# Kernel tuning notes

Measured on AMD Instinct MI355X. Metric: run time of the kernel, lower is better.

The kernel has to match this reference:

```python
import jax, jax.numpy as jnp
import numpy as np

NW, OBS, HS, HS2, HM, CTX, ACT = 2048, 512, 512, 512, 256, 128, 18


def setup_inputs() -> dict:
    key = jax.random.key(0)
    ks = jax.random.split(key, 20)
    s = 0.02  # small init so tanh/softmax/sigmoid stay in sane range
    f32 = jnp.float32
    return {
        "obs": jax.random.normal(ks[0], (NW, 1, OBS), f32),
        "hidden_memory": jax.random.normal(ks[1], (1, NW, HM), f32),
        # fnn: Linear(obs_size, hidden_size)
        "W1": (jax.random.normal(ks[2], (HS, OBS), f32) * s),
        "b1": jnp.zeros((HS,), f32),
        # context: Linear(hidden_memory_size + 1, context_size)
        "Wc": (jax.random.normal(ks[3], (CTX, HM + 1), f32) * s),
        "bc": jnp.zeros((CTX,), f32),
        # attention: Linear(context_size, 1)
        "Wa": (jax.random.normal(ks[4], (1, CTX), f32) * s),
        "ba": jnp.zeros((1,), f32),
        # GRU(input=1, hidden=HM)
        "W_ih": (jax.random.normal(ks[5], (3 * HM, 1), f32) * s),
        "b_ih": jnp.zeros((3 * HM,), f32),
        "W_hh": (jax.random.normal(ks[6], (3 * HM, HM), f32) * s),
        "b_hh": jnp.zeros((3 * HM,), f32),
        # fnn2: Linear(hidden_size + hidden_memory_size, hidden_size_2)
        "W2": (jax.random.normal(ks[7], (HS2, HS + HM), f32) * s),
        "b2": jnp.zeros((HS2,), f32),
        # actor / critic heads
        "Wact": (jax.random.normal(ks[8], (ACT, HS2), f32) * s),
        "bact": jnp.zeros((ACT,), f32),
        "Wcrit": (jax.random.normal(ks[9], (1, HS2), f32) * s),
        "bcrit": jnp.zeros((1,), f32),
    }


def reference(obs, hidden_memory, W1, b1, Wc, bc, Wa, ba,
              W_ih, b_ih, W_hh, b_hh, W2, b2, Wact, bact, Wcrit, bcrit):
    # obs: [NW, 1, OBS], hidden_memory: [1, NW, HM]
    feat = jax.nn.relu(jnp.einsum('bto,ho->bth', obs, W1) + b1)  # [NW,1,HS]

    # context: Linear([obs_scalar, hidden_memory]) + tanh.
    # Split the (HM+1)-dim contraction: col 0 multiplies the obs scalar,
    # cols 1: contract with the broadcast hidden memory (same math as the
    # torch cat + Linear, without materializing the [NW,1,OBS,HM+1] tensor).
    h = jnp.swapaxes(hidden_memory, 0, 1)                        # [NW,1,HM]
    h_term = jnp.einsum('btm,cm->btc', h, Wc[:, 1:]) + bc        # [NW,1,CTX]
    ctx = jnp.tanh(obs[..., None] * Wc[:, 0] + h_term[:, :, None, :])  # [NW,1,OBS,CTX]

    # attention: Linear(CTX -> 1) then softmax over the obs dimension (dim=-2
    # of [...,OBS,1] == OBS after squeeze)
    alog = jnp.einsum('btoc,c->bto', ctx, Wa[0]) + ba[0]         # [NW,1,OBS]
    attn = jax.nn.softmax(alog, axis=-1)
    dset = jnp.sum(attn * obs, axis=-1, keepdims=True)           # [NW,1,1]

    # single-step GRU (torch gate ordering: r, z, n)
    x = dset[:, 0, :]                                            # [NW,1]
    hp = hidden_memory[0]                                        # [NW,HM]
    gi = x @ W_ih.T + b_ih                                       # [NW,3HM]
    gh = hp @ W_hh.T + b_hh
    ir, iz, inn = jnp.split(gi, 3, axis=-1)
    hr, hz, hn = jnp.split(gh, 3, axis=-1)
    r = jax.nn.sigmoid(ir + hr)
    z = jax.nn.sigmoid(iz + hz)
    n = jnp.tanh(inn + r * hn)
    hnew = (1.0 - z) * n + z * hp                                # [NW,HM]

    out = jnp.concatenate([feat[:, 0, :], hnew], axis=-1)        # [NW,HS+HM]
    out = jax.nn.relu(out @ W2.T + b2)                           # [NW,HS2]
    logits = out @ Wact.T + bact                                 # [NW,ACT]
    action = jax.random.categorical(jax.random.key(42), logits)  # [NW]
    log_prob = jax.nn.log_softmax(logits)[jnp.arange(logits.shape[0]), action]
    value = out @ Wcrit.T + bcrit                                # [NW,1]
    return (action, value, log_prob)
```

## Files before the change

kernel.cpp:

```cpp
#include <hip/hip_runtime.h>
#include <stdint.h>

#define NW   2048
#define OBS  512
#define HS   512
#define HS2  512
#define HM   256
#define CTX  128
#define ACT  18

#define K2LE 2.8853900817779268f

#define W1T_OFF   0
#define WCT_OFF   262144
#define W2T_OFF   294912
#define WHHQ_OFF  688128
#define FEAT_OFF  950272
#define GATES_OFF 1998848
#define HTERM_OFF 3571712
#define X_OFF     3833856

#if __has_builtin(__builtin_amdgcn_exp2f)
#define EXP2F(x) __builtin_amdgcn_exp2f(x)
#else
#define EXP2F(x) exp2f(x)
#endif
#if __has_builtin(__builtin_amdgcn_rcpf)
#define RCPF(x) __builtin_amdgcn_rcpf(x)
#else
#define RCPF(x) (1.0f/(x))
#endif

#define TFR(x0, x1, R) { x0 += x1; x1 = (x1 << R) | (x1 >> (32 - R)); x1 ^= x0; }

__device__ __forceinline__ void threefry_0_42(uint32_t x0, uint32_t x1,
                                              uint32_t& o0, uint32_t& o1) {
    const uint32_t ks0 = 0u;
    const uint32_t ks1 = 42u;
    const uint32_t ks2 = 0x1BD11BDAu ^ ks0 ^ ks1;
    x0 += ks0; x1 += ks1;
    TFR(x0, x1, 13) TFR(x0, x1, 15) TFR(x0, x1, 26) TFR(x0, x1, 6)
    x0 += ks1; x1 += ks2 + 1u;
    TFR(x0, x1, 17) TFR(x0, x1, 29) TFR(x0, x1, 16) TFR(x0, x1, 24)
    x0 += ks2; x1 += ks0 + 2u;
    TFR(x0, x1, 13) TFR(x0, x1, 15) TFR(x0, x1, 26) TFR(x0, x1, 6)
    x0 += ks0; x1 += ks1 + 3u;
    TFR(x0, x1, 17) TFR(x0, x1, 29) TFR(x0, x1, 16) TFR(x0, x1, 24)
    x0 += ks1; x1 += ks2 + 4u;
    TFR(x0, x1, 13) TFR(x0, x1, 15) TFR(x0, x1, 26) TFR(x0, x1, 6)
    x0 += ks2; x1 += ks0 + 5u;
    o0 = x0; o1 = x1;
}

__device__ __forceinline__ float gumbel_ra(int row, int a) {
    uint32_t n = (uint32_t)(row * ACT + a);
    uint32_t o0, o1;
    threefry_0_42(0u, n, o0, o1);
    uint32_t bits = o0 ^ o1;
    uint32_t fb = (bits >> 9) | 0x3F800000u;
    float f = __uint_as_float(fb) - 1.0f;
    const float tiny = 1.17549435e-38f;
    float u = (f < tiny) ? tiny : f;
    return -logf(-logf(u));
}

__device__ __forceinline__ float fast_tanh(float x) {
    float e = __expf(2.0f * x);
    return 1.0f - 2.0f / (e + 1.0f);
}
__device__ __forceinline__ float fast_sig(float x) {
    return 1.0f / (1.0f + __expf(-x));
}

__global__ __launch_bounds__(256) void transpose_weights(
    const float* __restrict__ W1, const float* __restrict__ Wc,
    const float* __restrict__ Whh, const float* __restrict__ W2,
    float* __restrict__ ws)
{
    __shared__ float t[3][32][33];
    const int tx = threadIdx.x & 31, ty = threadIdx.x >> 5;
    int b = blockIdx.x;
    if (b < 672) {
        const float* src; float* dst; int ld, off, R, it, jt;
        if (b < 256)      { src = W1;  dst = ws + W1T_OFF;  ld = 512; off = 0; it = b >> 4; jt = b & 15; R = 512; }
        else if (b < 288) { int bb = b - 256; src = Wc;  dst = ws + WCT_OFF;  ld = 257; off = 1; it = bb >> 3; jt = bb & 7;  R = 128; }
        else              { int bb = b - 288; src = W2;  dst = ws + W2T_OFF;  ld = 768; off = 0; it = bb / 24; jt = bb % 24; R = 512; }
        const int i0 = it * 32, j0 = jt * 32;
        #pragma unroll
        for (int q = 0; q < 4; ++q)
            t[0][ty + 8 * q][tx] = src[(i0 + ty + 8 * q) * ld + off + j0 + tx];
        __syncthreads();
        #pragma unroll
        for (int q = 0; q < 4; ++q)
            dst[(j0 + ty + 8 * q) * R + i0 + tx] = t[0][tx][ty + 8 * q];
    } else {
        int bb = b - 672;
        const int mt = bb >> 3, jt = bb & 7;
        const int m0 = mt * 32, j0 = jt * 32;
        #pragma unroll
        for (int g = 0; g < 3; ++g)
            #pragma unroll
            for (int q = 0; q < 4; ++q)
                t[g][ty + 8 * q][tx] = Whh[(g * HM + j0 + ty + 8 * q) * HM + m0 + tx];
        __syncthreads();
        float4* dst = (float4*)(ws + WHHQ_OFF);
        #pragma unroll
        for (int q = 0; q < 4; ++q) {
            int ml = ty + 8 * q, jl = tx;
            dst[(size_t)(m0 + ml) * HM + j0 + jl] =
                make_float4(t[0][jl][ml], t[1][jl][ml], t[2][jl][ml], 0.0f);
        }
    }
}

__global__ __launch_bounds__(256) void gemm8(
    const float* __restrict__ obs, const float* __restrict__ hmem,
    const float* __restrict__ b1,  const float* __restrict__ bc,
    const float* __restrict__ bhh, float* __restrict__ ws)
{
    __shared__ float s_act[8 * 512];
    const int tid = threadIdx.x;
    const int wv = tid >> 6, lane = tid & 63;
    const int bid = blockIdx.x;

    if (bid < 256) {
        const int m0 = bid * 8;
        for (int i = tid; i < 1024; i += 256) {
            int r = i >> 7, kq = i & 127;
            *(float4*)&s_act[r * 512 + kq * 4] =
                *(const float4*)&obs[(size_t)(m0 + r) * 512 + kq * 4];
        }
        __syncthreads();
        const float2* __restrict__ Wt = (const float2*)(ws + W1T_OFF);
        const int c2 = wv * 64 + lane;
        float2 acc[8];
        #pragma unroll
        for (int r = 0; r < 8; ++r) acc[r] = make_float2(0.f, 0.f);
        #pragma unroll 4
        for (int k = 0; k < 512; k += 4) {
            float2 w0 = Wt[(k + 0) * 256 + c2];
            float2 w1 = Wt[(k + 1) * 256 + c2];
            float2 w2 = Wt[(k + 2) * 256 + c2];
            float2 w3 = Wt[(k + 3) * 256 + c2];
            #pragma unroll
            for (int r = 0; r < 8; ++r) {
                float4 o = *(const float4*)&s_act[r * 512 + k];
                acc[r].x = fmaf(o.x, w0.x, acc[r].x); acc[r].y = fmaf(o.x, w0.y, acc[r].y);
                acc[r].x = fmaf(o.y, w1.x, acc[r].x); acc[r].y = fmaf(o.y, w1.y, acc[r].y);
                acc[r].x = fmaf(o.z, w2.x, acc[r].x); acc[r].y = fmaf(o.z, w2.y, acc[r].y);
                acc[r].x = fmaf(o.w, w3.x, acc[r].x); acc[r].y = fmaf(o.w, w3.y, acc[r].y);
            }
        }
        float2 bb = ((const float2*)b1)[c2];
        float* F = ws + FEAT_OFF;
        #pragma unroll
        for (int r = 0; r < 8; ++r) {
            float2 v;
            v.x = fmaxf(acc[r].x + bb.x, 0.f);
            v.y = fmaxf(acc[r].y + bb.y, 0.f);
            *(float2*)&F[(size_t)(m0 + r) * 512 + c2 * 2] = v;
        }
    } else if (bid < 512) {
        const int m0 = (bid - 256) * 8;
        for (int i = tid; i < 512; i += 256) {
            int r = i >> 6, kq = i & 63;
            *(float4*)&s_act[r * 256 + kq * 4] =
                *(const float4*)&hmem[(size_t)(m0 + r) * 256 + kq * 4];
        }
        __syncthreads();
        const float4* __restrict__ Q = (const float4*)(ws + WHHQ_OFF);
        const int j = wv * 64 + lane;
        float ar[8] = {0,0,0,0,0,0,0,0}, az[8] = {0,0,0,0,0,0,0,0}, an[8] = {0,0,0,0,0,0,0,0};
        #pragma unroll 4
        for (int k = 0; k < 256; k += 4) {
            float4 q0 = Q[(k + 0) * 256 + j];
            float4 q1 = Q[(k + 1) * 256 + j];
            float4 q2 = Q[(k + 2) * 256 + j];
            float4 q3 = Q[(k + 3) * 256 + j];
            #pragma unroll
            for (int r = 0; r < 8; ++r) {
                float4 h = *(const float4*)&s_act[r * 256 + k];
                ar[r] = fmaf(h.x, q0.x, ar[r]); az[r] = fmaf(h.x, q0.y, az[r]); an[r] = fmaf(h.x, q0.z, an[r]);
                ar[r] = fmaf(h.y, q1.x, ar[r]); az[r] = fmaf(h.y, q1.y, az[r]); an[r] = fmaf(h.y, q1.z, an[r]);
                ar[r] = fmaf(h.z, q2.x, ar[r]); az[r] = fmaf(h.z, q2.y, az[r]); an[r] = fmaf(h.z, q2.z, an[r]);
                ar[r] = fmaf(h.w, q3.x, ar[r]); az[r] = fmaf(h.w, q3.y, az[r]); an[r] = fmaf(h.w, q3.z, an[r]);
            }
        }
        float br = bhh[j], bz = bhh[HM + j], bn = bhh[2 * HM + j];
        float* G = ws + GATES_OFF;
        #pragma unroll
        for (int r = 0; r < 8; ++r) {
            size_t base = (size_t)(m0 + r) * 768 + j;
            G[base]       = ar[r] + br;
            G[base + 256] = az[r] + bz;
            G[base + 512] = an[r] + bn;
        }
    } else {
        const int m0 = (bid - 512) * 8;
        for (int i = tid; i < 512; i += 256) {
            int r = i >> 6, kq = i & 63;
            *(float4*)&s_act[r * 256 + kq * 4] =
                *(const float4*)&hmem[(size_t)(m0 + r) * 256 + kq * 4];
        }
        __syncthreads();
        const float2* __restrict__ Wt = (const float2*)(ws + WCT_OFF);
        const int r0 = wv * 2;
        float2 a0 = make_float2(0.f, 0.f), a1 = make_float2(0.f, 0.f);
        #pragma unroll 4
        for (int k = 0; k < 256; k += 4) {
            float2 w0 = Wt[(k + 0) * 64 + lane];
            float2 w1 = Wt[(k + 1) * 64 + lane];
            float2 w2 = Wt[(k + 2) * 64 + lane];
            float2 w3 = Wt[(k + 3) * 64 + lane];
            float4 o0 = *(const float4*)&s_act[r0 * 256 + k];
            float4 o1 = *(const float4*)&s_act[(r0 + 1) * 256 + k];
            a0.x = fmaf(o0.x, w0.x, a0.x); a0.y = fmaf(o0.x, w0.y, a0.y);
            a0.x = fmaf(o0.y, w1.x, a0.x); a0.y = fmaf(o0.y, w1.y, a0.y);
            a0.x = fmaf(o0.z, w2.x, a0.x); a0.y = fmaf(o0.z, w2.y, a0.y);
            a0.x = fmaf(o0.w, w3.x, a0.x); a0.y = fmaf(o0.w, w3.y, a0.y);
            a1.x = fmaf(o1.x, w0.x, a1.x); a1.y = fmaf(o1.x, w0.y, a1.y);
            a1.x = fmaf(o1.y, w1.x, a1.x); a1.y = fmaf(o1.y, w1.y, a1.y);
            a1.x = fmaf(o1.z, w2.x, a1.x); a1.y = fmaf(o1.z, w2.y, a1.y);
            a1.x = fmaf(o1.w, w3.x, a1.x); a1.y = fmaf(o1.w, w3.y, a1.y);
        }
        float2 bb = ((const float2*)bc)[lane];
        float* H = ws + HTERM_OFF;
        float2 v0, v1;
        v0.x = K2LE * (a0.x + bb.x); v0.y = K2LE * (a0.y + bb.y);
        v1.x = K2LE * (a1.x + bb.x); v1.y = K2LE * (a1.y + bb.y);
        *(float2*)&H[(size_t)(m0 + r0) * 128 + lane * 2]     = v0;
        *(float2*)&H[(size_t)(m0 + r0 + 1) * 128 + lane * 2] = v1;
    }
}

__global__ __launch_bounds__(512) void attn_kernel(
    const float* __restrict__ obs, const float* __restrict__ Wc,
    const float* __restrict__ Wa,  const float* __restrict__ ba,
    float* __restrict__ ws)
{
    __shared__ float s_obs[4][512];
    __shared__ float s_ht[4][128];
    __shared__ float s_alog[4][512];
    __shared__ float s_wc0[128], s_wa2[128];

    const int tid = threadIdx.x;
    const int row0 = blockIdx.x * 4;
    const float* hterm = ws + HTERM_OFF;
    float* X = ws + X_OFF;

    {
        int r = tid >> 7, kq = tid & 127;
        *(float4*)&s_obs[r][kq * 4] =
            *(const float4*)&obs[(size_t)(row0 + r) * 512 + kq * 4];
    }
    if (tid < 128) {
        int r = tid >> 5, kq = tid & 31;
        *(float4*)&s_ht[r][kq * 4] =
            *(const float4*)&hterm[(size_t)(row0 + r) * 128 + kq * 4];
    } else if (tid < 256) {
        int t = tid - 128;
        s_wc0[t] = K2LE * Wc[t * (HM + 1)];
        s_wa2[t] = 2.0f * Wa[t];
    }
    __syncthreads();

    {
        const float ba0 = ba[0];
        const int o = tid;
        float ob[4], acA[4];
        #pragma unroll
        for (int r = 0; r < 4; ++r) { ob[r] = s_obs[r][o]; acA[r] = 0.f; }
        float swa = 0.f;
        for (int c = 0; c < 128; c += 4) {
            float4 v = *(const float4*)&s_wa2[c];
            swa += v.x + v.y + v.z + v.w;
        }
        swa *= 0.5f;
        for (int c4 = 0; c4 < 32; ++c4) {
            float4 wc = *(const float4*)&s_wc0[c4 * 4];
            float4 wa = *(const float4*)&s_wa2[c4 * 4];
            #pragma unroll
            for (int r = 0; r < 4; ++r) {
                float4 ht = *(const float4*)&s_ht[r][c4 * 4];
                float t0 = fmaf(ob[r], wc.x, ht.x);
                acA[r] = fmaf(wa.x, RCPF(EXP2F(t0) + 1.f), acA[r]);
                float t1 = fmaf(ob[r], wc.y, ht.y);
                acA[r] = fmaf(wa.y, RCPF(EXP2F(t1) + 1.f), acA[r]);
                float t2 = fmaf(ob[r], wc.z, ht.z);
                acA[r] = fmaf(wa.z, RCPF(EXP2F(t2) + 1.f), acA[r]);
                float t3 = fmaf(ob[r], wc.w, ht.w);
                acA[r] = fmaf(wa.w, RCPF(EXP2F(t3) + 1.f), acA[r]);
            }
        }
        #pragma unroll
        for (int r = 0; r < 4; ++r) s_alog[r][o] = ba0 + swa - acA[r];
    }
    __syncthreads();

    {
        const int wv = tid >> 6, lane = tid & 63;
        if (wv < 4) {
            const int r = wv;
            float m = -1e30f;
            for (int o = lane; o < 512; o += 64) m = fmaxf(m, s_alog[r][o]);
            #pragma unroll
            for (int d = 32; d >= 1; d >>= 1) m = fmaxf(m, __shfl_xor(m, d));
            float se = 0.f, sw = 0.f;
            for (int o = lane; o < 512; o += 64) {
                float e = __expf(s_alog[r][o] - m);
                se += e; sw += e * s_obs[r][o];
            }
            #pragma unroll
            for (int d = 32; d >= 1; d >>= 1) { se += __shfl_xor(se, d); sw += __shfl_xor(sw, d); }
            if (lane == 0) X[row0 + r] = sw / se;
        }
    }
}

__global__ __launch_bounds__(512) void out2_heads(
    const float* __restrict__ hmem,  const float* __restrict__ W_ih,
    const float* __restrict__ b_ih,  const float* __restrict__ b2,
    const float* __restrict__ Wact,  const float* __restrict__ bact,
    const float* __restrict__ Wcrit, const float* __restrict__ bcrit,
    const float* __restrict__ ws,    float* __restrict__ out)
{
    __shared__ float s_act[8 * 768];
    __shared__ float s_P[8 * 512];
    const int tid = threadIdx.x;
    const int wv = tid >> 6, lane = tid & 63;
    const int m0 = blockIdx.x * 8;
    const float* F = ws + FEAT_OFF;
    const float* G = ws + GATES_OFF;
    const float* X = ws + X_OFF;

    for (int i = tid; i < 1024; i += 512) {
        int r = i >> 7, kq = i & 127;
        *(float4*)&s_act[r * 768 + kq * 4] =
            *(const float4*)&F[(size_t)(m0 + r) * 512 + kq * 4];
    }
    for (int i = tid; i < 2048; i += 512) {
        int r = i >> 8, j = i & 255;
        int grow = m0 + r;
        float g0 = G[(size_t)grow * 768 + j];
        float g1 = G[(size_t)grow * 768 + 256 + j];
        float g2 = G[(size_t)grow * 768 + 512 + j];
        float hp = hmem[(size_t)grow * 256 + j];
        float x  = X[grow];
        float rg = fast_sig(fmaf(x, W_ih[j], b_ih[j]) + g0);
        float zg = fast_sig(fmaf(x, W_ih[256 + j], b_ih[256 + j]) + g1);
        float ng = fast_tanh(fmaf(x, W_ih[512 + j], b_ih[512 + j]) + rg * g2);
        s_act[r * 768 + 512 + j] = (1.0f - zg) * ng + zg * hp;
    }
    __syncthreads();

    const float2* __restrict__ Wt = (const float2*)(ws + W2T_OFF);
    const int kg = wv & 1, cg = wv >> 1;
    const int c2 = cg * 64 + lane;
    const int k0 = kg * 384;
    float2 acc[8];
    #pragma unroll
    for (int r = 0; r < 8; ++r) acc[r] = make_float2(0.f, 0.f);
    #pragma unroll 4
    for (int k = k0; k < k0 + 384; k += 4) {
        float2 w0 = Wt[(k + 0) * 256 + c2];
        float2 w1 = Wt[(k + 1) * 256 + c2];
        float2 w2 = Wt[(k + 2) * 256 + c2];
        float2 w3 = Wt[(k + 3) * 256 + c2];
        #pragma unroll
        for (int r = 0; r < 8; ++r) {
            float4 o = *(const float4*)&s_act[r * 768 + k];
            acc[r].x = fmaf(o.x, w0.x, acc[r].x); acc[r].y = fmaf(o.x, w0.y, acc[r].y);
            acc[r].x = fmaf(o.y, w1.x, acc[r].x); acc[r].y = fmaf(o.y, w1.y, acc[r].y);
            acc[r].x = fmaf(o.z, w2.x, acc[r].x); acc[r].y = fmaf(o.z, w2.y, acc[r].y);
            acc[r].x = fmaf(o.w, w3.x, acc[r].x); acc[r].y = fmaf(o.w, w3.y, acc[r].y);
        }
    }
    float2* P2 = (float2*)s_P;
    if (kg == 1) {
        #pragma unroll
        for (int r = 0; r < 8; ++r) P2[r * 256 + c2] = acc[r];
    }
    __syncthreads();
    float (*s_out)[512] = (float (*)[512])s_act;
    if (kg == 0) {
        float2 bb = ((const float2*)b2)[c2];
        #pragma unroll
        for (int r = 0; r < 8; ++r) {
            float2 p = P2[r * 256 + c2];
            float2 v;
            v.x = fmaxf(acc[r].x + p.x + bb.x, 0.f);
            v.y = fmaxf(acc[r].y + p.y + bb.y, 0.f);
            *(float2*)&s_out[r][c2 * 2] = v;
        }
    }
    __syncthreads();

    {
        const int rr = wv;
        const int grow = m0 + rr;
        float4 x0 = *(const float4*)&s_out[rr][lane * 8];
        float4 x1 = *(const float4*)&s_out[rr][lane * 8 + 4];
        float la[ACT];
        #pragma unroll
        for (int a = 0; a < ACT; ++a) {
            const float4* wa4 = (const float4*)&Wact[a * HS2 + lane * 8];
            float4 w0 = wa4[0], w1 = wa4[1];
            float p = x0.x * w0.x + x0.y * w0.y + x0.z * w0.z + x0.w * w0.w
                    + x1.x * w1.x + x1.y * w1.y + x1.z * w1.z + x1.w * w1.w;
            #pragma unroll
            for (int d = 32; d >= 1; d >>= 1) p += __shfl_xor(p, d);
            la[a] = p + bact[a];
        }
        const float4* wc4 = (const float4*)&Wcrit[lane * 8];
        float4 w0 = wc4[0], w1 = wc4[1];
        float pv = x0.x * w0.x + x0.y * w0.y + x0.z * w0.z + x0.w * w0.w
                 + x1.x * w1.x + x1.y * w1.y + x1.z * w1.z + x1.w * w1.w;
        #pragma unroll
        for (int d = 32; d >= 1; d >>= 1) pv += __shfl_xor(pv, d);

        float g = (lane < ACT) ? gumbel_ra(grow, lane) : 0.0f;
        float best = -1e30f; int amax = 0;
        float mx = -1e30f;
        #pragma unroll
        for (int a = 0; a < ACT; ++a) {
            float g_ = __shfl(g, a);
            float y = la[a] + g_;
            if (y > best) { best = y; amax = a; }
            mx = fmaxf(mx, la[a]);
        }
        float se = 0.f;
        #pragma unroll
        for (int a = 0; a < ACT; ++a) se += __expf(la[a] - mx);
        float lse = mx + logf(se);
        float lp = la[amax] - lse;
        if (lane == 0) {
            out[grow]          = (float)amax;
            out[NW + grow]     = pv + bcrit[0];
            out[2 * NW + grow] = lp;
        }
    }
}

extern "C" void kernel_launch(void* const* d_in, const int* in_sizes, int n_in,
                              void* d_out, int out_size, void* d_ws, size_t ws_size,
                              hipStream_t stream) {
    const float* obs   = (const float*)d_in[0];
    const float* hmem  = (const float*)d_in[1];
    const float* W1    = (const float*)d_in[2];
    const float* b1    = (const float*)d_in[3];
    const float* Wc    = (const float*)d_in[4];
    const float* bc    = (const float*)d_in[5];
    const float* Wa    = (const float*)d_in[6];
    const float* ba    = (const float*)d_in[7];
    const float* W_ih  = (const float*)d_in[8];
    const float* b_ih  = (const float*)d_in[9];
    const float* W_hh  = (const float*)d_in[10];
    const float* b_hh  = (const float*)d_in[11];
    const float* W2    = (const float*)d_in[12];
    const float* b2    = (const float*)d_in[13];
    const float* Wact  = (const float*)d_in[14];
    const float* bact  = (const float*)d_in[15];
    const float* Wcrit = (const float*)d_in[16];
    const float* bcrit = (const float*)d_in[17];
    float* ws = (float*)d_ws;

    transpose_weights<<<736, 256, 0, stream>>>(W1, Wc, W_hh, W2, ws);
    gemm8<<<768, 256, 0, stream>>>(obs, hmem, b1, bc, b_hh, ws);
    attn_kernel<<<512, 512, 0, stream>>>(obs, Wc, Wa, ba, ws);
    out2_heads<<<256, 512, 0, stream>>>(hmem, W_ih, b_ih, b2,
                                        Wact, bact, Wcrit, bcrit, ws, (float*)d_out);
}
```

Before: 125.8 us.

## Split out2 GEMM from heads and widen grid with column and K splitting

Measured after the change: 119.2 us. -5.3%, faster.

```diff
diff --git a/kernel.cpp b/kernel.cpp
--- a/kernel.cpp
+++ b/kernel.cpp
@@ -19,6 +19,7 @@
 #define GATES_OFF 1998848
 #define HTERM_OFF 3571712
 #define X_OFF     3833856
+#define OUT2_OFF  3835904
 
 #if __has_builtin(__builtin_amdgcn_exp2f)
 #define EXP2F(x) __builtin_amdgcn_exp2f(x)
@@ -317,21 +318,20 @@
     }
 }
 
-__global__ __launch_bounds__(512) void out2_heads(
+__global__ __launch_bounds__(512) void out2_gemm(
     const float* __restrict__ hmem,  const float* __restrict__ W_ih,
     const float* __restrict__ b_ih,  const float* __restrict__ b2,
-    const float* __restrict__ Wact,  const float* __restrict__ bact,
-    const float* __restrict__ Wcrit, const float* __restrict__ bcrit,
-    const float* __restrict__ ws,    float* __restrict__ out)
+    const float* __restrict__ ws_c,  float* __restrict__ ws)
 {
     __shared__ float s_act[8 * 768];
-    __shared__ float s_P[8 * 512];
+    __shared__ float s_P[6144];
     const int tid = threadIdx.x;
     const int wv = tid >> 6, lane = tid & 63;
-    const int m0 = blockIdx.x * 8;
-    const float* F = ws + FEAT_OFF;
-    const float* G = ws + GATES_OFF;
-    const float* X = ws + X_OFF;
+    const int rowb = blockIdx.x >> 1, colb = blockIdx.x & 1;
+    const int m0 = rowb * 8;
+    const float* F = ws_c + FEAT_OFF;
+    const float* G = ws_c + GATES_OFF;
+    const float* X = ws_c + X_OFF;
 
     for (int i = tid; i < 1024; i += 512) {
         int r = i >> 7, kq = i & 127;
@@ -353,15 +353,15 @@
     }
     __syncthreads();
 
-    const float2* __restrict__ Wt = (const float2*)(ws + W2T_OFF);
-    const int kg = wv & 1, cg = wv >> 1;
-    const int c2 = cg * 64 + lane;
-    const int k0 = kg * 384;
+    const float2* __restrict__ Wt = (const float2*)(ws_c + W2T_OFF);
+    const int kg = wv & 3, cg = wv >> 2;
+    const int c2 = colb * 128 + cg * 64 + lane;
+    const int k0 = kg * 192;
     float2 acc[8];
     #pragma unroll
     for (int r = 0; r < 8; ++r) acc[r] = make_float2(0.f, 0.f);
     #pragma unroll 4
-    for (int k = k0; k < k0 + 384; k += 4) {
+    for (int k = k0; k < k0 + 192; k += 4) {
         float2 w0 = Wt[(k + 0) * 256 + c2];
         float2 w1 = Wt[(k + 1) * 256 + c2];
         float2 w2 = Wt[(k + 2) * 256 + c2];
@@ -376,68 +376,78 @@
         }
     }
     float2* P2 = (float2*)s_P;
-    if (kg == 1) {
-        #pragma unroll
-        for (int r = 0; r < 8; ++r) P2[r * 256 + c2] = acc[r];
+    const int cl = cg * 64 + lane;
+    if (kg != 0) {
+        #pragma unroll
+        for (int r = 0; r < 8; ++r) P2[((kg - 1) * 8 + r) * 128 + cl] = acc[r];
     }
     __syncthreads();
-    float (*s_out)[512] = (float (*)[512])s_act;
     if (kg == 0) {
         float2 bb = ((const float2*)b2)[c2];
+        float* O = ws + OUT2_OFF;
         #pragma unroll
         for (int r = 0; r < 8; ++r) {
-            float2 p = P2[r * 256 + c2];
+            float2 p0 = P2[(0 * 8 + r) * 128 + cl];
+            float2 p1 = P2[(1 * 8 + r) * 128 + cl];
+            float2 p2 = P2[(2 * 8 + r) * 128 + cl];
             float2 v;
-            v.x = fmaxf(acc[r].x + p.x + bb.x, 0.f);
-            v.y = fmaxf(acc[r].y + p.y + bb.y, 0.f);
-            *(float2*)&s_out[r][c2 * 2] = v;
-        }
-    }
-    __syncthreads();
-
-    {
-        const int rr = wv;
-        const int grow = m0 + rr;
-        float4 x0 = *(const float4*)&s_out[rr][lane * 8];
-        float4 x1 = *(const float4*)&s_out[rr][lane * 8 + 4];
-        float la[ACT];
-        #pragma unroll
-        for (int a = 0; a < ACT; ++a) {
-            const float4* wa4 = (const float4*)&Wact[a * HS2 + lane * 8];
-            float4 w0 = wa4[0], w1 = wa4[1];
-            float p = x0.x * w0.x + x0.y * w0.y + x0.z * w0.z + x0.w * w0.w
-                    + x1.x * w1.x + x1.y * w1.y + x1.z * w1.z + x1.w * w1.w;
-            #pragma unroll
-            for (int d = 32; d >= 1; d >>= 1) p += __shfl_xor(p, d);
-            la[a] = p + bact[a];
-        }
-        const float4* wc4 = (const float4*)&Wcrit[lane * 8];
-        float4 w0 = wc4[0], w1 = wc4[1];
-        float pv = x0.x * w0.x + x0.y * w0.y + x0.z * w0.z + x0.w * w0.w
-                 + x1.x * w1.x + x1.y * w1.y + x1.z * w1.z + x1.w * w1.w;
-        #pragma unroll
-        for (int d = 32; d >= 1; d >>= 1) pv += __shfl_xor(pv, d);
-
-        float g = (lane < ACT) ? gumbel_ra(grow, lane) : 0.0f;
-        float best = -1e30f; int amax = 0;
-        float mx = -1e30f;
-        #pragma unroll
-        for (int a = 0; a < ACT; ++a) {
-            float g_ = __shfl(g, a);
-            float y = la[a] + g_;
-            if (y > best) { best = y; amax = a; }
-            mx = fmaxf(mx, la[a]);
-        }
-        float se = 0.f;
-        #pragma unroll
-        for (int a = 0; a < ACT; ++a) se += __expf(la[a] - mx);
-        float lse = mx + logf(se);
-        float lp = la[amax] - lse;
-        if (lane == 0) {
-            out[grow]          = (float)amax;
-            out[NW + grow]     = pv + bcrit[0];
-            out[2 * NW + grow] = lp;
-        }
+            v.x = fmaxf(acc[r].x + p0.x + p1.x + p2.x + bb.x, 0.f);
+            v.y = fmaxf(acc[r].y + p0.y + p1.y + p2.y + bb.y, 0.f);
+            *(float2*)&ws[OUT2_OFF + (size_t)(m0 + r) * 512 + c2 * 2] = v;
+        }
+        (void)O;
+    }
+}
+
+__global__ __launch_bounds__(512) void heads_kernel(
+    const float* __restrict__ Wact,  const float* __restrict__ bact,
+    const float* __restrict__ Wcrit, const float* __restrict__ bcrit,
+    const float* __restrict__ ws,    float* __restrict__ out)
+{
+    const int wv = threadIdx.x >> 6, lane = threadIdx.x & 63;
+    const int grow = blockIdx.x * 8 + wv;
+    const float* o2 = ws + OUT2_OFF;
+
+    float4 x0 = *(const float4*)&o2[(size_t)grow * 512 + lane * 8];
+    float4 x1 = *(const float4*)&o2[(size_t)grow * 512 + lane * 8 + 4];
+
+    float la[ACT];
+    #pragma unroll
+    for (int a = 0; a < ACT; ++a) {
+        const float4* wa4 = (const float4*)&Wact[a * HS2 + lane * 8];
+        float4 w0 = wa4[0], w1 = wa4[1];
+        float p = x0.x * w0.x + x0.y * w0.y + x0.z * w0.z + x0.w * w0.w
+                + x1.x * w1.x + x1.y * w1.y + x1.z * w1.z + x1.w * w1.w;
+        #pragma unroll
+        for (int d = 32; d >= 1; d >>= 1) p += __shfl_xor(p, d);
+        la[a] = p + bact[a];
+    }
+    const float4* wc4 = (const float4*)&Wcrit[lane * 8];
+    float4 w0 = wc4[0], w1 = wc4[1];
+    float pv = x0.x * w0.x + x0.y * w0.y + x0.z * w0.z + x0.w * w0.w
+             + x1.x * w1.x + x1.y * w1.y + x1.z * w1.z + x1.w * w1.w;
+    #pragma unroll
+    for (int d = 32; d >= 1; d >>= 1) pv += __shfl_xor(pv, d);
+
+    float g = (lane < ACT) ? gumbel_ra(grow, lane) : 0.0f;
+    float best = -1e30f; int amax = 0;
+    float mx = -1e30f;
+    #pragma unroll
+    for (int a = 0; a < ACT; ++a) {
+        float g_ = __shfl(g, a);
+        float y = la[a] + g_;
+        if (y > best) { best = y; amax = a; }
+        mx = fmaxf(mx, la[a]);
+    }
+    float se = 0.f;
+    #pragma unroll
+    for (int a = 0; a < ACT; ++a) se += __expf(la[a] - mx);
+    float lse = mx + logf(se);
+    float lp = la[amax] - lse;
+    if (lane == 0) {
+        out[grow]          = (float)amax;
+        out[NW + grow]     = pv + bcrit[0];
+        out[2 * NW + grow] = lp;
     }
 }
 
@@ -467,6 +477,6 @@
     transpose_weights<<<736, 256, 0, stream>>>(W1, Wc, W_hh, W2, ws);
     gemm8<<<768, 256, 0, stream>>>(obs, hmem, b1, bc, b_hh, ws);
     attn_kernel<<<512, 512, 0, stream>>>(obs, Wc, Wa, ba, ws);
-    out2_heads<<<256, 512, 0, stream>>>(hmem, W_ih, b_ih, b2,
-                                        Wact, bact, Wcrit, bcrit, ws, (float*)d_out);
-}
+    out2_gemm<<<512, 512, 0, stream>>>(hmem, W_ih, b_ih, b2, ws, ws);
+    heads_kernel<<<256, 512, 0, stream>>>(Wact, bact, Wcrit, bcrit, ws, (float*)d_out);
+}
```
